# Kernel tuning notes

Hardware: AMD Instinct MI355X
Metric: run time of the kernel (lower is better)

Reference implementation:

```python
import jax, jax.numpy as jnp
import numpy as np

NEG_SLOPE = 0.01  # nn.LeakyReLU default


def setup_inputs() -> dict:
    key = jax.random.key(0)
    k1, k2, k3, k4, k5 = jax.random.split(key, 5)
    SLI, FEAT, NODE = 8, 64, 20000
    N = SLI * NODE          # 160000 graph nodes
    E = 2_560_000           # avg degree 16
    OUT = 64
    inputs = jax.random.normal(k1, (SLI, FEAT, NODE), dtype=jnp.float32)
    src = jax.random.randint(k2, (E,), 0, N, dtype=jnp.int64)
    dst = jax.random.randint(k3, (E,), 0, N, dtype=jnp.int64)
    # GraphConv params (glorot-ish scale)
    W = jax.random.normal(k4, (FEAT, OUT), dtype=jnp.float32) / np.sqrt(FEAT)
    b = jnp.zeros((OUT,), dtype=jnp.float32)
    return {"inputs": inputs, "W": W, "b": b, "src": src, "dst": dst}


def reference(inputs, W, b, src, dst):
    # inputs: [sli, feat, node] -> [sli*node, feat]  (dropout is eval-mode identity)
    sli, feat, node = inputs.shape
    x = jnp.transpose(inputs, (0, 2, 1)).reshape(-1, feat)
    N = sli * node
    ones = jnp.ones(src.shape, dtype=x.dtype)
    deg_out = jax.ops.segment_sum(ones, src, num_segments=N)  # out-degree of src
    deg_in = jax.ops.segment_sum(ones, dst, num_segments=N)   # in-degree of dst
    norm_src = jnp.where(deg_out > 0, deg_out, 1.0) ** -0.5
    norm_dst = jnp.where(deg_in > 0, deg_in, 1.0) ** -0.5
    # norm='both': scale src feats, sum-aggregate over edges, scale dst
    h = x * norm_src[:, None]
    agg = jax.ops.segment_sum(h[src], dst, num_segments=N)    # [N, feat]
    agg = agg * norm_dst[:, None]
    out = agg @ W + b                                          # [N, out]
    out = jax.nn.leaky_relu(out, NEG_SLOPE)
    # [N, out] -> [sli, node, out] -> [sli, out, node]
    return jnp.transpose(out.reshape(sli, node, -1), (0, 2, 1))
```

## Files before the change

kernel.cpp:

```cpp
#include <hip/hip_runtime.h>
#include <hip/hip_bf16.h>

constexpr int SLI  = 8;
constexpr int FEAT = 64;
constexpr int NODE = 20000;
constexpr int NTOT = SLI * NODE;
constexpr int OUTF = 64;
constexpr int CAP  = 48;
constexpr int NBD  = 625;
constexpr int NBS  = 313;
constexpr int BCAPD = 4864;
constexpr int BCAPS = 8960;
constexpr int EPB  = 4096;
constexpr int NDST = NTOT / 256;

typedef __attribute__((ext_vector_type(8))) short bf16x8;
typedef __attribute__((ext_vector_type(4))) float f32x4;

static __device__ inline unsigned short f2bf(float x) {
    unsigned u = __float_as_uint(x);
    unsigned r = (u + 0x7fffu + ((u >> 16) & 1u)) >> 16;
    return (unsigned short)r;
}

__global__ __launch_bounds__(512) void k_part(const int* __restrict__ src,
                                              const int* __restrict__ dst,
                                              int* __restrict__ cursor_d,
                                              unsigned* __restrict__ bucket_d,
                                              int* __restrict__ cursor_s,
                                              unsigned short* __restrict__ bucket_s, int E) {
    __shared__ unsigned       svalD[EPB];
    __shared__ unsigned short sbktD[EPB];
    __shared__ unsigned sS[EPB];
    __shared__ int histD[NBD], lcurD[NBD], baseD[NBD];
    __shared__ int histS[NBS], lcurS[NBS], baseS[NBS];
    __shared__ int goffD[64], goffS[64];
    int t  = threadIdx.x;
    int e0 = blockIdx.x * EPB;
    for (int i = t; i < NBD; i += 512) histD[i] = 0;
    for (int i = t; i < NBS; i += 512) histS[i] = 0;
    __syncthreads();
    int myS[8], myD[8];
#pragma unroll
    for (int i = 0; i < 2; ++i) {
        int j  = (e0 >> 2) + i * 512 + t;
        int b4 = j << 2;
        if (b4 + 3 < E) {
            int4 vs = ((const int4*)src)[j];
            int4 vd = ((const int4*)dst)[j];
            myS[4*i+0] = vs.x; myS[4*i+1] = vs.y; myS[4*i+2] = vs.z; myS[4*i+3] = vs.w;
            myD[4*i+0] = vd.x; myD[4*i+1] = vd.y; myD[4*i+2] = vd.z; myD[4*i+3] = vd.w;
        } else {
#pragma unroll
            for (int c = 0; c < 4; ++c) {
                int idx = b4 + c;
                myS[4*i+c] = (idx < E) ? src[idx] : -1;
                myD[4*i+c] = (idx < E) ? dst[idx] : -1;
            }
        }
    }
#pragma unroll
    for (int i = 0; i < 8; ++i) {
        if (myD[i] >= 0) {
            atomicAdd(&histD[myD[i] >> 8], 1);
            atomicAdd(&histS[myS[i] >> 9], 1);
        }
    }
    __syncthreads();
    int rbD[2], rbS0;
#pragma unroll
    for (int i = 0; i < 2; ++i) {
        int bb = t + i * 512;
        rbD[i] = (bb < NBD) ? atomicAdd(&cursor_d[bb], histD[bb]) : 0;
    }
    rbS0 = (t < NBS) ? atomicAdd(&cursor_s[t], histS[t]) : 0;
    int wv = t >> 6, ln = t & 63;
    if (wv == 0) {
        int b0 = ln * 10, s = 0;
#pragma unroll
        for (int j = 0; j < 10; ++j) { int bb = b0 + j; if (bb < NBD) s += histD[bb]; }
        int x = s;
        for (int off = 1; off < 64; off <<= 1) {
            int y = __shfl_up(x, off, 64);
            if (ln >= off) x += y;
        }
        goffD[ln] = x - s;
    } else if (wv == 1) {
        int b0 = ln * 5, s = 0;
#pragma unroll
        for (int j = 0; j < 5; ++j) { int bb = b0 + j; if (bb < NBS) s += histS[bb]; }
        int x = s;
        for (int off = 1; off < 64; off <<= 1) {
            int y = __shfl_up(x, off, 64);
            if (ln >= off) x += y;
        }
        goffS[ln] = x - s;
    }
    asm volatile("s_waitcnt lgkmcnt(0)\n\ts_barrier" ::: "memory");
    for (int bb = t; bb < NBD; bb += 512) {
        int g = bb / 10;
        int sD = goffD[g];
        for (int k = g * 10; k < bb; ++k) sD += histD[k];
        lcurD[bb] = sD;
    }
    for (int bb = t; bb < NBS; bb += 512) {
        int g = bb / 5;
        int sS2 = goffS[g];
        for (int k = g * 5; k < bb; ++k) sS2 += histS[k];
        lcurS[bb] = sS2;
    }
    asm volatile("s_waitcnt lgkmcnt(0)\n\ts_barrier" ::: "memory");
#pragma unroll
    for (int i = 0; i < 8; ++i) {
        if (myD[i] >= 0) {
            int bD = myD[i] >> 8;
            int p  = atomicAdd(&lcurD[bD], 1);
            svalD[p] = ((unsigned)(myD[i] & 255) << 18) | (unsigned)myS[i];
            sbktD[p] = (unsigned short)bD;
            int bS = myS[i] >> 9;
            int q  = atomicAdd(&lcurS[bS], 1);
            sS[q] = ((unsigned)bS << 9) | (unsigned)(myS[i] & 511);
        }
    }
#pragma unroll
    for (int i = 0; i < 2; ++i) { int bb = t + i * 512; if (bb < NBD) baseD[bb] = rbD[i]; }
    if (t < NBS) baseS[t] = rbS0;
    __syncthreads();
    int nval = E - e0; if (nval > EPB) nval = EPB;
    for (int p = t; p < nval; p += 512) {
        int bD = sbktD[p];
        int wi = baseD[bD] + (p - (lcurD[bD] - histD[bD]));
        if (wi < BCAPD) bucket_d[(size_t)bD * BCAPD + wi] = svalD[p];
        unsigned vs = sS[p];
        int bS = vs >> 9;
        int wj = baseS[bS] + (p - (lcurS[bS] - histS[bS]));
        if (wj < BCAPS) bucket_s[(size_t)bS * BCAPS + wj] = (unsigned short)(vs & 511);
    }
}

__global__ __launch_bounds__(512) void k_fin(const int* __restrict__ cursor_d,
                                             const unsigned* __restrict__ bucket_d,
                                             const int* __restrict__ cursor_s,
                                             const unsigned short* __restrict__ bucket_s,
                                             int* __restrict__ col_ell,
                                             int* __restrict__ deg_in,
                                             int* __restrict__ deg_out) {
    __shared__ char lds[256 * CAP * 4 + 2048];
    int t = threadIdx.x;
    if (blockIdx.x < NBS) {
        int* cnt = (int*)lds;
        int b = blockIdx.x;
        cnt[t] = 0;
        __syncthreads();
        int len = cursor_s[b]; if (len > BCAPS) len = BCAPS;
        const unsigned short* p = bucket_s + (size_t)b * BCAPS;
        for (int i = t; i < len; i += 512)
            atomicAdd(&cnt[p[i]], 1);
        __syncthreads();
        int n0 = b << 9;
        if (n0 + t < NTOT) deg_out[n0 + t] = cnt[t];
    } else {
        int* ell = (int*)lds;
        int* cnt = (int*)(lds + 256 * CAP * 4);
        int b = blockIdx.x - NBS;
        if (t < 256) cnt[t] = 0;
        __syncthreads();
        int len = cursor_d[b]; if (len > BCAPD) len = BCAPD;
        const unsigned* p = bucket_d + (size_t)b * BCAPD;
        for (int i = t; i < len; i += 512) {
            unsigned e = p[i];
            int r = (e >> 18) & 255;
            int pos = atomicAdd(&cnt[r], 1);
            if (pos < CAP) ell[r * CAP + pos] = (int)(e & 0x3FFFFu);
        }
        __syncthreads();
        int node0 = b << 8;
        if (t < 256) deg_in[node0 + t] = cnt[t];
        size_t gbase = (size_t)node0 * CAP;
        const int4* lsrc = (const int4*)ell;
        int4* gdst = (int4*)(col_ell + gbase);
#pragma unroll
        for (int i = 0; i < 6; ++i)
            gdst[i * 512 + t] = lsrc[i * 512 + t];
    }
}

__global__ __launch_bounds__(256) void k_transpose(const float* __restrict__ in,
                                                   const int* __restrict__ deg_out,
                                                   unsigned short* __restrict__ xs) {
    __shared__ float tile[64][65];
    int sli = blockIdx.y;
    int n0  = blockIdx.x * 64;
    int t   = threadIdx.x;
    int fx  = t & 15;
    int fr  = t >> 4;
    const float* ip = in + (size_t)sli * FEAT * NODE;
    int nq = n0 + fx * 4;
#pragma unroll
    for (int i = 0; i < 4; ++i) {
        int f = fr + i * 16;
        float4 v = {0.f, 0.f, 0.f, 0.f};
        if (nq < NODE) v = *(const float4*)(ip + (size_t)f * NODE + nq);
        tile[f][fx * 4 + 0] = v.x;
        tile[f][fx * 4 + 1] = v.y;
        tile[f][fx * 4 + 2] = v.z;
        tile[f][fx * 4 + 3] = v.w;
    }
    __syncthreads();
    int h  = t & 31;
    int nr = t >> 5;
#pragma unroll
    for (int i = 0; i < 8; ++i) {
        int nl   = nr + i * 8;
        int node = n0 + nl;
        if (node < NODE) {
            int n = sli * NODE + node;
            int d = deg_out[n];
            float sc = rsqrtf(d > 0 ? (float)d : 1.f);
            unsigned lo = f2bf(tile[2 * h][nl] * sc);
            unsigned hi = f2bf(tile[2 * h + 1][nl] * sc);
            *(unsigned*)(xs + (size_t)n * 64 + 2 * h) = lo | (hi << 16);
        }
    }
}

__global__ __launch_bounds__(256) void k_agg_gemm(const int* __restrict__ deg_in,
                                                  const int* __restrict__ col_ell,
                                                  const unsigned short* __restrict__ xs,
                                                  const float* __restrict__ W,
                                                  const float* __restrict__ b,
                                                  float* __restrict__ out) {
    __shared__ char lds[18432];
    unsigned short* av = (unsigned short*)lds;
    unsigned short* wt = (unsigned short*)(lds + 9216);
    float (*otile)[65] = (float(*)[65])lds;

    int t    = threadIdx.x;
    int lane = t & 63;
    int w    = t >> 6;
    int g8   = lane >> 3;
    int f8   = lane & 7;
    int sli  = blockIdx.y;
    int n0   = blockIdx.x * 64;

#pragma unroll
    for (int i = 0; i < 16; ++i) {
        int idx = i * 256 + t;
        int f = idx >> 6, o = idx & 63;
        wt[o * 72 + f] = f2bf(W[idx]);
    }

    int m0 = w * 16;
    for (int ii = 0; ii < 16; ii += 2) {
        int rowA = m0 + ii, rowB = rowA + 1;
        int nodeA = n0 + rowA, nodeB = n0 + rowB;
        int nA = sli * NODE + nodeA, nB = sli * NODE + nodeB;
        int dA = (nodeA < NODE) ? deg_in[nA] : 0;
        int dB = (nodeB < NODE) ? deg_in[nB] : 0;
        int degA = dA < CAP ? dA : CAP;
        int degB = dB < CAP ? dB : CAP;
        int cA = (lane < degA) ? col_ell[(size_t)nA * CAP + lane] : NTOT;
        int cB = (lane < degB) ? col_ell[(size_t)nB * CAP + lane] : NTOT;
        float accA[8] = {0,0,0,0,0,0,0,0};
        float accB[8] = {0,0,0,0,0,0,0,0};
        int gmax = degA > degB ? degA : degB;
        int groups = (gmax + 7) >> 3;
#pragma unroll 2
        for (int j = 0; j < groups; ++j) {
            int idx = 8 * j + g8;
            int sA = __shfl(cA, idx, 64);
            int sB = __shfl(cB, idx, 64);
            uint4 vA = *(const uint4*)(xs + (size_t)sA * 64 + f8 * 8);
            uint4 vB = *(const uint4*)(xs + (size_t)sB * 64 + f8 * 8);
            accA[0] += __uint_as_float(vA.x << 16);
            accA[1] += __uint_as_float(vA.x & 0xffff0000u);
            accA[2] += __uint_as_float(vA.y << 16);
            accA[3] += __uint_as_float(vA.y & 0xffff0000u);
            accA[4] += __uint_as_float(vA.z << 16);
            accA[5] += __uint_as_float(vA.z & 0xffff0000u);
            accA[6] += __uint_as_float(vA.w << 16);
            accA[7] += __uint_as_float(vA.w & 0xffff0000u);
            accB[0] += __uint_as_float(vB.x << 16);
            accB[1] += __uint_as_float(vB.x & 0xffff0000u);
            accB[2] += __uint_as_float(vB.y << 16);
            accB[3] += __uint_as_float(vB.y & 0xffff0000u);
            accB[4] += __uint_as_float(vB.z << 16);
            accB[5] += __uint_as_float(vB.z & 0xffff0000u);
            accB[6] += __uint_as_float(vB.w << 16);
            accB[7] += __uint_as_float(vB.w & 0xffff0000u);
        }
#pragma unroll
        for (int k = 0; k < 8; ++k) {
            accA[k] += __shfl_xor(accA[k], 8, 64);
            accA[k] += __shfl_xor(accA[k], 16, 64);
            accA[k] += __shfl_xor(accA[k], 32, 64);
            accB[k] += __shfl_xor(accB[k], 8, 64);
            accB[k] += __shfl_xor(accB[k], 16, 64);
            accB[k] += __shfl_xor(accB[k], 32, 64);
        }
        if (g8 == 0) {
            float scA = rsqrtf(dA > 0 ? (float)dA : 1.f);
            float scB = rsqrtf(dB > 0 ? (float)dB : 1.f);
            uint4 hv;
            hv.x = (unsigned)f2bf(accA[0] * scA) | ((unsigned)f2bf(accA[1] * scA) << 16);
            hv.y = (unsigned)f2bf(accA[2] * scA) | ((unsigned)f2bf(accA[3] * scA) << 16);
            hv.z = (unsigned)f2bf(accA[4] * scA) | ((unsigned)f2bf(accA[5] * scA) << 16);
            hv.w = (unsigned)f2bf(accA[6] * scA) | ((unsigned)f2bf(accA[7] * scA) << 16);
            ((uint4*)(av + rowA * 72))[f8] = hv;
            hv.x = (unsigned)f2bf(accB[0] * scB) | ((unsigned)f2bf(accB[1] * scB) << 16);
            hv.y = (unsigned)f2bf(accB[2] * scB) | ((unsigned)f2bf(accB[3] * scB) << 16);
            hv.z = (unsigned)f2bf(accB[4] * scB) | ((unsigned)f2bf(accB[5] * scB) << 16);
            hv.w = (unsigned)f2bf(accB[6] * scB) | ((unsigned)f2bf(accB[7] * scB) << 16);
            ((uint4*)(av + rowB * 72))[f8] = hv;
        }
    }

    __syncthreads();

    int q = lane >> 4, r16 = lane & 15;
    bf16x8 afr[2], bfr[4][2];
#pragma unroll
    for (int ks = 0; ks < 2; ++ks)
        afr[ks] = *(const bf16x8*)(av + (m0 + r16) * 72 + ks * 32 + q * 8);
#pragma unroll
    for (int nt = 0; nt < 4; ++nt)
#pragma unroll
        for (int ks = 0; ks < 2; ++ks)
            bfr[nt][ks] = *(const bf16x8*)(wt + (nt * 16 + r16) * 72 + ks * 32 + q * 8);

    f32x4 acc4[4];
#pragma unroll
    for (int nt = 0; nt < 4; ++nt) acc4[nt] = (f32x4){0.f, 0.f, 0.f, 0.f};
#pragma unroll
    for (int nt = 0; nt < 4; ++nt)
#pragma unroll
        for (int ks = 0; ks < 2; ++ks)
            acc4[nt] = __builtin_amdgcn_mfma_f32_16x16x32_bf16(afr[ks], bfr[nt][ks], acc4[nt], 0, 0, 0);
    __syncthreads();

#pragma unroll
    for (int nt = 0; nt < 4; ++nt) {
        int oc = nt * 16 + r16;
        float bias = b[oc];
#pragma unroll
        for (int r = 0; r < 4; ++r) {
            float v = acc4[nt][r] + bias;
            v = v > 0.f ? v : 0.01f * v;
            otile[oc][m0 + q * 4 + r] = v;
        }
    }
    __syncthreads();

    const size_t obase = (size_t)sli * OUTF * NODE;
#pragma unroll
    for (int i = 0; i < 16; ++i) {
        int o    = w + i * 4;
        int node = n0 + lane;
        if (node < NODE)
            out[obase + (size_t)o * NODE + node] = otile[o][lane];
    }
}

extern "C" void kernel_launch(void* const* d_in, const int* in_sizes, int n_in,
                              void* d_out, int out_size, void* d_ws, size_t ws_size,
                              hipStream_t stream) {
    const float* inputs = (const float*)d_in[0];
    const float* W      = (const float*)d_in[1];
    const float* b      = (const float*)d_in[2];
    const int*   src    = (const int*)d_in[3];
    const int*   dst    = (const int*)d_in[4];
    float*       out    = (float*)d_out;
    const int E = in_sizes[3];

    char* ws = (char*)d_ws;
    int* deg_out = (int*)ws;
    int* deg_in  = (int*)(ws + (size_t)NTOT * 4);
    int* col_ell = (int*)(ws + (size_t)2 * NTOT * 4);
    char* R      = (char*)col_ell + (size_t)NTOT * CAP * 4;
    unsigned*       bucket_d = (unsigned*)R;
    unsigned short* bucket_s = (unsigned short*)(R + (size_t)NBD * BCAPD * 4);
    int*            cursors  = (int*)(R + (size_t)NBD * BCAPD * 4 + (size_t)NBS * BCAPS * 2);
    int* cursor_d = cursors;
    int* cursor_s = cursors + NBD;
    unsigned short* xs = (unsigned short*)R;

    hipMemsetAsync(cursors, 0, (size_t)(NBD + NBS) * 4, stream);
    hipMemsetAsync(xs + (size_t)NTOT * 64, 0, 64 * sizeof(unsigned short), stream);

    int PB = (E + EPB - 1) / EPB;
    k_part<<<PB, 512, 0, stream>>>(src, dst, cursor_d, bucket_d, cursor_s, bucket_s, E);

    k_fin<<<NBS + NDST, 512, 0, stream>>>(cursor_d, bucket_d, cursor_s, bucket_s,
                                          col_ell, deg_in, deg_out);

    dim3 tgrid((NODE + 63) / 64, SLI);
    k_transpose<<<tgrid, 256, 0, stream>>>(inputs, deg_out, xs);

    k_agg_gemm<<<tgrid, 256, 0, stream>>>(deg_in, col_ell, xs, W, b, out);
}
```

Before: 224.5 us.

## Split out-degree pass and fuse transpose into destination-ELL build kernel

```diff
diff --git a/kernel.cpp b/kernel.cpp
--- a/kernel.cpp
+++ b/kernel.cpp
@@ -9,10 +9,11 @@
 constexpr int CAP  = 48;
 constexpr int NBD  = 625;
 constexpr int NBS  = 313;
-constexpr int BCAPD = 4864;
+constexpr int BCAPD = 4608;
 constexpr int BCAPS = 8960;
 constexpr int EPB  = 4096;
 constexpr int NDST = NTOT / 256;
+constexpr int NTB  = 313 * SLI;
 
 typedef __attribute__((ext_vector_type(8))) short bf16x8;
 typedef __attribute__((ext_vector_type(4))) float f32x4;
@@ -138,31 +139,35 @@
     }
 }
 
-__global__ __launch_bounds__(512) void k_fin(const int* __restrict__ cursor_d,
-                                             const unsigned* __restrict__ bucket_d,
-                                             const int* __restrict__ cursor_s,
-                                             const unsigned short* __restrict__ bucket_s,
-                                             int* __restrict__ col_ell,
-                                             int* __restrict__ deg_in,
-                                             int* __restrict__ deg_out) {
+__global__ __launch_bounds__(512) void k_finS(const int* __restrict__ cursor_s,
+                                              const unsigned short* __restrict__ bucket_s,
+                                              int* __restrict__ deg_out) {
+    __shared__ int cnt[512];
+    int t = threadIdx.x, b = blockIdx.x;
+    cnt[t] = 0;
+    __syncthreads();
+    int len = cursor_s[b]; if (len > BCAPS) len = BCAPS;
+    const unsigned short* p = bucket_s + (size_t)b * BCAPS;
+    for (int i = t; i < len; i += 512)
+        atomicAdd(&cnt[p[i]], 1);
+    __syncthreads();
+    int n0 = b << 9;
+    if (n0 + t < NTOT) deg_out[n0 + t] = cnt[t];
+}
+
+__global__ __launch_bounds__(512) void k_fin2(const int* __restrict__ cursor_d,
+                                              const unsigned* __restrict__ bucket_d,
+                                              int* __restrict__ col_ell,
+                                              int* __restrict__ deg_in,
+                                              const float* __restrict__ in,
+                                              const int* __restrict__ deg_out,
+                                              unsigned short* __restrict__ xs) {
     __shared__ char lds[256 * CAP * 4 + 2048];
     int t = threadIdx.x;
-    if (blockIdx.x < NBS) {
-        int* cnt = (int*)lds;
-        int b = blockIdx.x;
-        cnt[t] = 0;
-        __syncthreads();
-        int len = cursor_s[b]; if (len > BCAPS) len = BCAPS;
-        const unsigned short* p = bucket_s + (size_t)b * BCAPS;
-        for (int i = t; i < len; i += 512)
-            atomicAdd(&cnt[p[i]], 1);
-        __syncthreads();
-        int n0 = b << 9;
-        if (n0 + t < NTOT) deg_out[n0 + t] = cnt[t];
-    } else {
+    if (blockIdx.x < NDST) {
         int* ell = (int*)lds;
         int* cnt = (int*)(lds + 256 * CAP * 4);
-        int b = blockIdx.x - NBS;
+        int b = blockIdx.x;
         if (t < 256) cnt[t] = 0;
         __syncthreads();
         int len = cursor_d[b]; if (len > BCAPD) len = BCAPD;
@@ -182,44 +187,40 @@
 #pragma unroll
         for (int i = 0; i < 6; ++i)
             gdst[i * 512 + t] = lsrc[i * 512 + t];
-    }
-}
-
-__global__ __launch_bounds__(256) void k_transpose(const float* __restrict__ in,
-                                                   const int* __restrict__ deg_out,
-                                                   unsigned short* __restrict__ xs) {
-    __shared__ float tile[64][65];
-    int sli = blockIdx.y;
-    int n0  = blockIdx.x * 64;
-    int t   = threadIdx.x;
-    int fx  = t & 15;
-    int fr  = t >> 4;
-    const float* ip = in + (size_t)sli * FEAT * NODE;
-    int nq = n0 + fx * 4;
-#pragma unroll
-    for (int i = 0; i < 4; ++i) {
-        int f = fr + i * 16;
-        float4 v = {0.f, 0.f, 0.f, 0.f};
-        if (nq < NODE) v = *(const float4*)(ip + (size_t)f * NODE + nq);
-        tile[f][fx * 4 + 0] = v.x;
-        tile[f][fx * 4 + 1] = v.y;
-        tile[f][fx * 4 + 2] = v.z;
-        tile[f][fx * 4 + 3] = v.w;
-    }
-    __syncthreads();
-    int h  = t & 31;
-    int nr = t >> 5;
-#pragma unroll
-    for (int i = 0; i < 8; ++i) {
-        int nl   = nr + i * 8;
-        int node = n0 + nl;
-        if (node < NODE) {
-            int n = sli * NODE + node;
-            int d = deg_out[n];
-            float sc = rsqrtf(d > 0 ? (float)d : 1.f);
-            unsigned lo = f2bf(tile[2 * h][nl] * sc);
-            unsigned hi = f2bf(tile[2 * h + 1][nl] * sc);
-            *(unsigned*)(xs + (size_t)n * 64 + 2 * h) = lo | (hi << 16);
+    } else {
+        float (*tile)[65] = (float(*)[65])lds;
+        int tb  = blockIdx.x - NDST;
+        int sli = tb / 313, nblk = tb - sli * 313;
+        int n0  = nblk * 64;
+        const float* ip = in + (size_t)sli * FEAT * NODE;
+        int fx = t & 15;
+        int fr = t >> 4;
+        int nq = n0 + fx * 4;
+#pragma unroll
+        for (int i = 0; i < 2; ++i) {
+            int f = fr + i * 32;
+            float4 v = {0.f, 0.f, 0.f, 0.f};
+            if (nq < NODE) v = *(const float4*)(ip + (size_t)f * NODE + nq);
+            tile[f][fx * 4 + 0] = v.x;
+            tile[f][fx * 4 + 1] = v.y;
+            tile[f][fx * 4 + 2] = v.z;
+            tile[f][fx * 4 + 3] = v.w;
+        }
+        __syncthreads();
+        int h  = t & 31;
+        int nr = t >> 5;
+#pragma unroll
+        for (int i = 0; i < 4; ++i) {
+            int nl   = nr + i * 16;
+            int node = n0 + nl;
+            if (node < NODE) {
+                int n = sli * NODE + node;
+                int d = deg_out[n];
+                float sc = rsqrtf(d > 0 ? (float)d : 1.f);
+                unsigned lo = f2bf(tile[2 * h][nl] * sc);
+                unsigned hi = f2bf(tile[2 * h + 1][nl] * sc);
+                *(unsigned*)(xs + (size_t)n * 64 + 2 * h) = lo | (hi << 16);
+            }
         }
     }
 }
@@ -373,16 +374,21 @@
     const int E = in_sizes[3];
 
     char* ws = (char*)d_ws;
-    int* deg_out = (int*)ws;
-    int* deg_in  = (int*)(ws + (size_t)NTOT * 4);
-    int* col_ell = (int*)(ws + (size_t)2 * NTOT * 4);
-    char* R      = (char*)col_ell + (size_t)NTOT * CAP * 4;
-    unsigned*       bucket_d = (unsigned*)R;
-    unsigned short* bucket_s = (unsigned short*)(R + (size_t)NBD * BCAPD * 4);
-    int*            cursors  = (int*)(R + (size_t)NBD * BCAPD * 4 + (size_t)NBS * BCAPS * 2);
+    const size_t szXs    = (size_t)(NTOT + 1) * 64 * 2;
+    const size_t szDeg   = (size_t)NTOT * 4;
+    const size_t szEll   = (size_t)NTOT * CAP * 4;
+    const size_t szBd    = (size_t)NBD * BCAPD * 4;
+    const size_t szBs    = (size_t)NBS * BCAPS * 2;
+
+    unsigned short* xs       = (unsigned short*)ws;
+    int*            deg_in   = (int*)(ws + szXs);
+    int*            deg_out  = (int*)(ws + szXs + szDeg);
+    int*            col_ell  = (int*)(ws + szXs + 2 * szDeg);
+    unsigned*       bucket_d = (unsigned*)(ws + szXs + 2 * szDeg + szEll);
+    unsigned short* bucket_s = (unsigned short*)(ws + szXs + 2 * szDeg + szEll + szBd);
+    int*            cursors  = (int*)(ws + szXs + 2 * szDeg + szEll + szBd + szBs);
     int* cursor_d = cursors;
     int* cursor_s = cursors + NBD;
-    unsigned short* xs = (unsigned short*)R;
 
     hipMemsetAsync(cursors, 0, (size_t)(NBD + NBS) * 4, stream);
     hipMemsetAsync(xs + (size_t)NTOT * 64, 0, 64 * sizeof(unsigned short), stream);
@@ -390,11 +396,11 @@
     int PB = (E + EPB - 1) / EPB;
     k_part<<<PB, 512, 0, stream>>>(src, dst, cursor_d, bucket_d, cursor_s, bucket_s, E);
 
-    k_fin<<<NBS + NDST, 512, 0, stream>>>(cursor_d, bucket_d, cursor_s, bucket_s,
-                                          col_ell, deg_in, deg_out);
+    k_finS<<<NBS, 512, 0, stream>>>(cursor_s, bucket_s, deg_out);
+
+    k_fin2<<<NDST + NTB, 512, 0, stream>>>(cursor_d, bucket_d, col_ell, deg_in,
+                                           inputs, deg_out, xs);
 
     dim3 tgrid((NODE + 63) / 64, SLI);
-    k_transpose<<<tgrid, 256, 0, stream>>>(inputs, deg_out, xs);
-
     k_agg_gemm<<<tgrid, 256, 0, stream>>>(deg_in, col_ell, xs, W, b, out);
 }
```

Result: no change. 222.4 us, median of 2 (-1.0%).
